# Optimization experiments

Measured on AMD Instinct MI355X. Metric: run time of the kernel, lower is better.

Reference implementation:

```python
import jax, jax.numpy as jnp
import numpy as np

N = 50000   # nodes
E = 800000  # edges (avg degree 16)
D = 128     # input feature dim
H = 128     # hidden dim
C = 10      # num classes
G = 16      # graphs in batch


def setup_inputs() -> dict:
    key = jax.random.key(0)
    ks = jax.random.split(key, 12)
    def w(k, shape):
        return jax.random.normal(k, shape, jnp.float32) / np.sqrt(shape[0]).astype(np.float32)
    return {
        "h": jax.random.normal(ks[0], (N, D), jnp.float32),
        "src": jax.random.randint(ks[1], (E,), 0, N, jnp.int32),
        "dst": jax.random.randint(ks[2], (E,), 0, N, jnp.int32),
        "graph_ids": jnp.sort(jax.random.randint(ks[3], (N,), 0, G, jnp.int32)),
        "W1a": w(ks[4], (D, H)), "b1a": jnp.zeros((H,), jnp.float32),
        "W2a": w(ks[5], (H, H)), "b2a": jnp.zeros((H,), jnp.float32),
        "W1b": w(ks[6], (H, H)), "b1b": jnp.zeros((H,), jnp.float32),
        "W2b": w(ks[7], (H, H)), "b2b": jnp.zeros((H,), jnp.float32),
        "Wc1": w(ks[8], (H, H)), "bc1": jnp.zeros((H,), jnp.float32),
        "Wc2": w(ks[9], (H, C)), "bc2": jnp.zeros((C,), jnp.float32),
    }


def _gin_layer(h, src, dst, W1, b1, W2, b2):
    # GIN aggregation, eps=0: z_i = h_i + sum_{j in N(i)} h_j
    agg = jax.ops.segment_sum(h[src], dst, num_segments=N)
    z = h + agg
    # 2-layer MLP apply function with relu activation ('relu' arg of GINLayer)
    z = jax.nn.relu(z @ W1 + b1)
    return jax.nn.relu(z @ W2 + b2)


def reference(h, src, dst, graph_ids, W1a, b1a, W2a, b2a,
              W1b, b1b, W2b, b2b, Wc1, bc1, Wc2, bc2):
    h = _gin_layer(h, src, dst, W1a, b1a, W2a, b2a)   # [N, H]
    h = _gin_layer(h, src, dst, W1b, b1b, W2b, b2b)   # [N, H]
    # dgl.mean_nodes over the batched graph
    sums = jax.ops.segment_sum(h, graph_ids, num_segments=G)                # [G, H]
    cnts = jax.ops.segment_sum(jnp.ones((N, 1), h.dtype), graph_ids, num_segments=G)
    h_g = sums / jnp.maximum(cnts, 1.0)
    # cls MLP: linear -> relu -> linear (logits)
    out = jax.nn.relu(h_g @ Wc1 + bc1) @ Wc2 + bc2    # [G, C]
    return out
```

## Files before the change

kernel.cpp:

```cpp
#include <hip/hip_runtime.h>
#include <stdint.h>

#define NN 50000
#define EE 800000
#define DD 128
#define GG 16
#define CC 10
#define NBK 196
#define BCH 4096
#define SMAX 5120

typedef unsigned short u16;
typedef __bf16 bf16x8 __attribute__((ext_vector_type(8)));
typedef float f32x4 __attribute__((ext_vector_type(4)));

__device__ inline u16 f2bf(float f) {
    unsigned u = __float_as_uint(f);
    u = u + 0x7fffu + ((u >> 16) & 1u);
    return (u16)(u >> 16);
}
__device__ inline unsigned pack2(float a, float b) {
    return (unsigned)f2bf(a) | ((unsigned)f2bf(b) << 16);
}
__device__ inline float bf2f(unsigned bits16) { return __uint_as_float(bits16 << 16); }
__device__ inline void acc8(float* a, uint4 v) {
    a[0] += __uint_as_float(v.x << 16); a[1] += __uint_as_float(v.x & 0xffff0000u);
    a[2] += __uint_as_float(v.y << 16); a[3] += __uint_as_float(v.y & 0xffff0000u);
    a[4] += __uint_as_float(v.z << 16); a[5] += __uint_as_float(v.z & 0xffff0000u);
    a[6] += __uint_as_float(v.w << 16); a[7] += __uint_as_float(v.w & 0xffff0000u);
}
__device__ inline void mand(uint4& v, int p) {
    unsigned m = p ? 0xffffffffu : 0u;
    v.x &= m; v.y &= m; v.z &= m; v.w &= m;
}

#define PZ (GG * DD)
#define PC (NN * DD / 4)
#define PW (4 * DD * DD)
#define PTOT (PZ + PC + PW)

__global__ void prep_kernel(const float* __restrict__ h,
                            const float* __restrict__ a, const float* __restrict__ b,
                            const float* __restrict__ c, const float* __restrict__ d,
                            int* __restrict__ zbase, u16* __restrict__ H0,
                            u16* __restrict__ wt) {
    int i = blockIdx.x * 256 + threadIdx.x;
    if (i < PZ) { zbase[i] = 0; return; }
    i -= PZ;
    if (i < PC) {
        int j = i * 4;
        float4 v = *(const float4*)(h + j);
        ushort4 o;
        o.x = f2bf(v.x); o.y = f2bf(v.y); o.z = f2bf(v.z); o.w = f2bf(v.w);
        *(ushort4*)(H0 + j) = o;
        return;
    }
    i -= PC;
    if (i < PW) {
        int m = i >> 14, r = i & 16383, k = r >> 7, j = r & 127;
        const float* W = (m == 0) ? a : (m == 1) ? b : (m == 2) ? c : d;
        wt[(m << 14) + (j << 7) + k] = f2bf(W[(k << 7) + j]);
    }
}

__global__ __launch_bounds__(256) void sortP1_kernel(const int* __restrict__ dst,
                                                     int* __restrict__ counts) {
    __shared__ int hist[NBK];
    int b = blockIdx.x, t = threadIdx.x;
    for (int i = t; i < NBK; i += 256) hist[i] = 0;
    __syncthreads();
    int e0 = b * BCH, e1 = min(e0 + BCH, EE);
    for (int e = e0 + t; e < e1; e += 256) atomicAdd(&hist[dst[e] >> 8], 1);
    __syncthreads();
    for (int i = t; i < NBK; i += 256) counts[b * NBK + i] = hist[i];
}

__global__ __launch_bounds__(256) void sortP2_kernel(int* __restrict__ counts,
                                                     int* __restrict__ bbase,
                                                     const int* __restrict__ gids,
                                                     int* __restrict__ gstart) {
    __shared__ int tmp[256];
    int t = threadIdx.x;
    if (t <= GG) {
        int lo = 0, hi = NN;
        while (lo < hi) { int mid = (lo + hi) >> 1; if (gids[mid] < t) lo = mid + 1; else hi = mid; }
        gstart[t] = lo;
    }
    int s = 0;
    if (t < NBK) {
        for (int b = 0; b < NBK; b++) {
            int c = counts[b * NBK + t];
            counts[b * NBK + t] = s;
            s += c;
        }
    }
    tmp[t] = (t < NBK) ? s : 0;
    __syncthreads();
    for (int off = 1; off < 256; off <<= 1) {
        int x = (t >= off) ? tmp[t - off] : 0;
        __syncthreads();
        tmp[t] += x;
        __syncthreads();
    }
    int base = tmp[t] - ((t < NBK) ? s : 0);
    if (t < NBK) {
        bbase[t] = base;
        for (int b = 0; b < NBK; b++) counts[b * NBK + t] += base;
    }
    if (t == NBK - 1) bbase[NBK] = tmp[t];
}

__global__ __launch_bounds__(256) void sortP3_kernel(const int* __restrict__ src,
                                                     const int* __restrict__ dst,
                                                     const int* __restrict__ counts,
                                                     int* __restrict__ epack) {
    __shared__ int curs[NBK];
    int b = blockIdx.x, t = threadIdx.x;
    for (int i = t; i < NBK; i += 256) curs[i] = counts[b * NBK + i];
    __syncthreads();
    int e0 = b * BCH, e1 = min(e0 + BCH, EE);
    for (int e = e0 + t; e < e1; e += 256) {
        int d = dst[e], s = src[e];
        int p = atomicAdd(&curs[d >> 8], 1);
        epack[p] = (s << 8) | (d & 255);
    }
}

__global__ __launch_bounds__(256) void sortP4_kernel(const int* __restrict__ epack,
                                                     const int* __restrict__ bbase,
                                                     int* __restrict__ offs,
                                                     int* __restrict__ ssrc) {
    __shared__ int hist[256];
    __shared__ int curs[256];
    __shared__ int stage[SMAX];
    int j = blockIdx.x, t = threadIdx.x;
    int n0 = j << 8;
    int b0 = bbase[j], b1 = bbase[j + 1];
    hist[t] = 0;
    __syncthreads();
    for (int e = b0 + t; e < b1; e += 256) atomicAdd(&hist[epack[e] & 255], 1);
    __syncthreads();
    int deg = hist[t];
    for (int off = 1; off < 256; off <<= 1) {
        int x = (t >= off) ? hist[t - off] : 0;
        __syncthreads();
        hist[t] += x;
        __syncthreads();
    }
    int loff = hist[t] - deg;
    curs[t] = loff;
    if (n0 + t <= NN) offs[n0 + t] = b0 + loff;
    __syncthreads();
    for (int e = b0 + t; e < b1; e += 256) {
        int pk = epack[e];
        int p = atomicAdd(&curs[pk & 255], 1);
        stage[p] = pk >> 8;
    }
    __syncthreads();
    int n = b1 - b0;
    for (int i = t; i < n; i += 256) ssrc[b0 + i] = stage[i];
}

__global__ __launch_bounds__(256) void agg_kernel(
    const u16* __restrict__ Hin, const int* __restrict__ offs,
    const int* __restrict__ ssrc, u16* __restrict__ Z) {
    int gid = blockIdx.x * 32 + (threadIdx.x >> 3);
    int lid = threadIdx.x & 7;
    if (gid >= 2 * NN) return;
    int node = gid >> 1;
    int foff = (gid & 1) * 64 + lid * 8;
    const u16* base = Hin + foff;

    float acc[8] = {0.f, 0.f, 0.f, 0.f, 0.f, 0.f, 0.f, 0.f};
    uint4 vs = *(const uint4*)(base + (size_t)node * DD);
    int e0 = offs[node], e1 = offs[node + 1];
    acc8(acc, vs);

    int nch = (e1 - e0 + 7) >> 3;
    if (nch > 0) {
        int elast = e1 - 1;
        int i0 = ssrc[e0];
        int i1 = ssrc[min(e0 + 1, elast)];
        int i2 = ssrc[min(e0 + 2, elast)];
        int i3 = ssrc[min(e0 + 3, elast)];
        int i4 = ssrc[min(e0 + 4, elast)];
        int i5 = ssrc[min(e0 + 5, elast)];
        int i6 = ssrc[min(e0 + 6, elast)];
        int i7 = ssrc[min(e0 + 7, elast)];
        int eb = e0;
        for (int c = 0; c < nch; c++) {
            int ebn = eb + 8;
            int n0 = i0, n1 = i1, n2 = i2, n3 = i3, n4 = i4, n5 = i5, n6 = i6, n7 = i7;
            if (c + 1 < nch) {
                n0 = ssrc[ebn];
                n1 = ssrc[min(ebn + 1, elast)];
                n2 = ssrc[min(ebn + 2, elast)];
                n3 = ssrc[min(ebn + 3, elast)];
                n4 = ssrc[min(ebn + 4, elast)];
                n5 = ssrc[min(ebn + 5, elast)];
                n6 = ssrc[min(ebn + 6, elast)];
                n7 = ssrc[min(ebn + 7, elast)];
            }
            uint4 v0 = *(const uint4*)(base + (size_t)i0 * DD);
            uint4 v1 = *(const uint4*)(base + (size_t)i1 * DD);
            uint4 v2 = *(const uint4*)(base + (size_t)i2 * DD);
            uint4 v3 = *(const uint4*)(base + (size_t)i3 * DD);
            uint4 v4 = *(const uint4*)(base + (size_t)i4 * DD);
            uint4 v5 = *(const uint4*)(base + (size_t)i5 * DD);
            uint4 v6 = *(const uint4*)(base + (size_t)i6 * DD);
            uint4 v7 = *(const uint4*)(base + (size_t)i7 * DD);
            mand(v1, eb + 1 < e1); mand(v2, eb + 2 < e1); mand(v3, eb + 3 < e1);
            mand(v4, eb + 4 < e1); mand(v5, eb + 5 < e1); mand(v6, eb + 6 < e1);
            mand(v7, eb + 7 < e1);
            acc8(acc, v0); acc8(acc, v1); acc8(acc, v2); acc8(acc, v3);
            acc8(acc, v4); acc8(acc, v5); acc8(acc, v6); acc8(acc, v7);
            i0 = n0; i1 = n1; i2 = n2; i3 = n3; i4 = n4; i5 = n5; i6 = n6; i7 = n7;
            eb = ebn;
        }
    }
    uint4 o;
    o.x = pack2(acc[0], acc[1]); o.y = pack2(acc[2], acc[3]);
    o.z = pack2(acc[4], acc[5]); o.w = pack2(acc[6], acc[7]);
    *(uint4*)(Z + (size_t)node * DD + foff) = o;
}

__global__ __launch_bounds__(256) void mlp_kernel(
    const u16* __restrict__ Zin, const u16* __restrict__ Wt1, const float* __restrict__ b1,
    const u16* __restrict__ Wt2, const float* __restrict__ b2,
    u16* __restrict__ Hout) {
    __shared__ u16 zb[64][136];
    const int wave = threadIdx.x >> 6;
    const int lane = threadIdx.x & 63;
    const int m16 = lane & 15;
    const int quad = lane >> 4;
    const int row0 = blockIdx.x * 64 + wave * 16;

#pragma unroll
    for (int p = 0; p < 4; p++) {
        int idx = p * 64 + lane;
        int r = idx >> 4, ch = idx & 15;
        if (row0 + r < NN)
            *(uint4*)&zb[wave * 16 + r][ch * 8] = *(const uint4*)(Zin + (size_t)(row0 + r) * DD + ch * 8);
    }

    bf16x8 afr[4];
#pragma unroll
    for (int kk = 0; kk < 4; kk++)
        afr[kk] = *(const bf16x8*)&zb[wave * 16 + m16][kk * 32 + quad * 8];
    f32x4 acc[8];
#pragma unroll
    for (int nt = 0; nt < 8; nt++) acc[nt] = (f32x4){0.f, 0.f, 0.f, 0.f};
#pragma unroll
    for (int kk = 0; kk < 4; kk++) {
#pragma unroll
        for (int nt = 0; nt < 8; nt++) {
            bf16x8 bfr = *(const bf16x8*)(Wt1 + ((nt * 16 + m16) << 7) + kk * 32 + quad * 8);
            acc[nt] = __builtin_amdgcn_mfma_f32_16x16x32_bf16(afr[kk], bfr, acc[nt], 0, 0, 0);
        }
    }
#pragma unroll
    for (int nt = 0; nt < 8; nt++) {
        int col = nt * 16 + m16;
        float bias = b1[col];
#pragma unroll
        for (int r = 0; r < 4; r++) {
            float yv = acc[nt][r] + bias;
            yv = yv > 0.f ? yv : 0.f;
            zb[wave * 16 + quad * 4 + r][col] = f2bf(yv);
        }
    }

#pragma unroll
    for (int kk = 0; kk < 4; kk++)
        afr[kk] = *(const bf16x8*)&zb[wave * 16 + m16][kk * 32 + quad * 8];
#pragma unroll
    for (int nt = 0; nt < 8; nt++) acc[nt] = (f32x4){0.f, 0.f, 0.f, 0.f};
#pragma unroll
    for (int kk = 0; kk < 4; kk++) {
#pragma unroll
        for (int nt = 0; nt < 8; nt++) {
            bf16x8 bfr = *(const bf16x8*)(Wt2 + ((nt * 16 + m16) << 7) + kk * 32 + quad * 8);
            acc[nt] = __builtin_amdgcn_mfma_f32_16x16x32_bf16(afr[kk], bfr, acc[nt], 0, 0, 0);
        }
    }
#pragma unroll
    for (int nt = 0; nt < 8; nt++) {
        int col = nt * 16 + m16;
        float bias = b2[col];
#pragma unroll
        for (int r = 0; r < 4; r++) {
            float ov = acc[nt][r] + bias;
            ov = ov > 0.f ? ov : 0.f;
            zb[wave * 16 + quad * 4 + r][col] = f2bf(ov);
        }
    }
#pragma unroll
    for (int p = 0; p < 4; p++) {
        int idx = p * 64 + lane;
        int r = idx >> 4, ch = idx & 15;
        if (row0 + r < NN)
            *(uint4*)(Hout + (size_t)(row0 + r) * DD + ch * 8) = *(const uint4*)&zb[wave * 16 + r][ch * 8];
    }
}

__global__ void pool_kernel(const u16* __restrict__ H2, const int* __restrict__ gstart,
                            float* __restrict__ pool) {
    int g = blockIdx.x >> 5, q = blockIdx.x & 31;
    int f = threadIdx.x;
    int s = gstart[g], e = gstart[g + 1];
    float sum = 0.f;
    for (int n = s + q; n < e; n += 32) sum += bf2f(H2[(size_t)n * DD + f]);
    atomicAdd(&pool[g * DD + f], sum);
}

__global__ void cls_kernel(const float* __restrict__ pool, const int* __restrict__ gstart,
                           const float* __restrict__ Wc1, const float* __restrict__ bc1,
                           const float* __restrict__ Wc2, const float* __restrict__ bc2,
                           float* __restrict__ out) {
    __shared__ float hg[128];
    __shared__ float y1[128];
    int g = blockIdx.x;
    int t = threadIdx.x;
    int cnt = gstart[g + 1] - gstart[g];
    float inv = 1.f / (float)(cnt > 1 ? cnt : 1);
    hg[t] = pool[g * DD + t] * inv;
    __syncthreads();
    float a = bc1[t];
    for (int k = 0; k < DD; k++) a += hg[k] * Wc1[k * DD + t];
    y1[t] = a > 0.f ? a : 0.f;
    __syncthreads();
    if (t < CC) {
        float o = bc2[t];
        for (int k = 0; k < DD; k++) o += y1[k] * Wc2[k * CC + t];
        out[g * CC + t] = o;
    }
}

extern "C" void kernel_launch(void* const* d_in, const int* in_sizes, int n_in,
                              void* d_out, int out_size, void* d_ws, size_t ws_size,
                              hipStream_t stream) {
    const float* h    = (const float*)d_in[0];
    const int*   src  = (const int*)d_in[1];
    const int*   dst  = (const int*)d_in[2];
    const int*   gids = (const int*)d_in[3];
    const float* W1a  = (const float*)d_in[4];
    const float* b1a  = (const float*)d_in[5];
    const float* W2a  = (const float*)d_in[6];
    const float* b2a  = (const float*)d_in[7];
    const float* W1b  = (const float*)d_in[8];
    const float* b1b  = (const float*)d_in[9];
    const float* W2b  = (const float*)d_in[10];
    const float* b2b  = (const float*)d_in[11];
    const float* Wc1  = (const float*)d_in[12];
    const float* bc1  = (const float*)d_in[13];
    const float* Wc2  = (const float*)d_in[14];
    const float* bc2  = (const float*)d_in[15];
    float* out = (float*)d_out;

    char* ws = (char*)d_ws;
    u16*   H0     = (u16*)(ws);
    u16*   H1     = (u16*)(ws + 12800000);
    u16*   H2     = (u16*)(ws + 25600000);
    u16*   Wt     = (u16*)(ws + 38400000);
    float* pool   = (float*)(ws + 38531072);
    int*   offs   = (int*)(ws + 38539264);
    int*   ssrc   = (int*)(ws + 38739268);
    int*   gstart = (int*)(ws + 41939268);
    int*   counts = (int*)(ws + 41939336);
    int*   bbase  = (int*)(ws + 42093000);
    int*   epack  = (int*)(ws + 42093792);
    u16*   Z1     = H2;
    u16*   Z2     = H0;

    prep_kernel<<<dim3((PTOT + 255) / 256), dim3(256), 0, stream>>>(h, W1a, W2a, W1b, W2b, (int*)pool, H0, Wt);
    sortP1_kernel<<<dim3(NBK), dim3(256), 0, stream>>>(dst, counts);
    sortP2_kernel<<<dim3(1), dim3(256), 0, stream>>>(counts, bbase, gids, gstart);
    sortP3_kernel<<<dim3(NBK), dim3(256), 0, stream>>>(src, dst, counts, epack);
    sortP4_kernel<<<dim3(NBK), dim3(256), 0, stream>>>(epack, bbase, offs, ssrc);
    agg_kernel<<<dim3((2 * NN + 31) / 32), dim3(256), 0, stream>>>(H0, offs, ssrc, Z1);
    mlp_kernel<<<dim3((NN + 63) / 64), dim3(256), 0, stream>>>(Z1, Wt, b1a, Wt + 16384, b2a, H1);
    agg_kernel<<<dim3((2 * NN + 31) / 32), dim3(256), 0, stream>>>(H1, offs, ssrc, Z2);
    mlp_kernel<<<dim3((NN + 63) / 64), dim3(256), 0, stream>>>(Z2, Wt + 32768, b1b, Wt + 49152, b2b, H2);
    pool_kernel<<<dim3(GG * 32), dim3(128), 0, stream>>>(H2, gstart, pool);
    cls_kernel<<<dim3(GG), dim3(128), 0, stream>>>(pool, gstart, Wc1, bc1, Wc2, bc2, out);
}
```

Measured before the change: 305.6 us.

## Fuse histogram into prep kernel, transpose counts for parallel scan, add nontemporal memops

The bucket histogram pass now runs in the same launch as the fp32-to-bf16 conversion and weight transpose, which removes one kernel launch and lets the two run concurrently. The counts table is stored bucket-major, so the single-block scan can split it into contiguous chunks per thread instead of serially walking 196 strided entries per thread. Bucket bases are then read directly from counts, and the separate bbase array is dropped. Nontemporal loads and stores are also used for streaming feature tensors in the prep, aggregation and MLP kernels, which risks losing L2 reuse where the next kernel reads the same data.

```diff
diff --git a/kernel.cpp b/kernel.cpp
--- a/kernel.cpp
+++ b/kernel.cpp
@@ -9,10 +9,14 @@
 #define NBK 196
 #define BCH 4096
 #define SMAX 5120
+#define FT (NBK * NBK)
+#define CHK 151
 
 typedef unsigned short u16;
 typedef __bf16 bf16x8 __attribute__((ext_vector_type(8)));
 typedef float f32x4 __attribute__((ext_vector_type(4)));
+typedef unsigned int u32x4 __attribute__((ext_vector_type(4)));
+typedef float fl4 __attribute__((ext_vector_type(4)));
 
 __device__ inline u16 f2bf(float f) {
     unsigned u = __float_as_uint(f);
@@ -33,23 +37,50 @@
     unsigned m = p ? 0xffffffffu : 0u;
     v.x &= m; v.y &= m; v.z &= m; v.w &= m;
 }
+__device__ inline void nt_store16(void* p, uint4 v) {
+    u32x4 x; x.x = v.x; x.y = v.y; x.z = v.z; x.w = v.w;
+    __builtin_nontemporal_store(x, (u32x4*)p);
+}
+__device__ inline uint4 nt_load16(const void* p) {
+    u32x4 x = __builtin_nontemporal_load((const u32x4*)p);
+    uint4 r; r.x = x.x; r.y = x.y; r.z = x.z; r.w = x.w;
+    return r;
+}
+__device__ inline float4 nt_loadf4(const float* p) {
+    fl4 x = __builtin_nontemporal_load((const fl4*)p);
+    float4 r; r.x = x.x; r.y = x.y; r.z = x.z; r.w = x.w;
+    return r;
+}
 
 #define PZ (GG * DD)
 #define PC (NN * DD / 4)
 #define PW (4 * DD * DD)
 #define PTOT (PZ + PC + PW)
-
-__global__ void prep_kernel(const float* __restrict__ h,
-                            const float* __restrict__ a, const float* __restrict__ b,
-                            const float* __restrict__ c, const float* __restrict__ d,
-                            int* __restrict__ zbase, u16* __restrict__ H0,
-                            u16* __restrict__ wt) {
-    int i = blockIdx.x * 256 + threadIdx.x;
+#define PBLK ((PTOT + 255) / 256)
+
+__global__ __launch_bounds__(256) void prepsort_kernel(
+    const float* __restrict__ h,
+    const float* __restrict__ a, const float* __restrict__ b,
+    const float* __restrict__ c, const float* __restrict__ d,
+    int* __restrict__ zbase, u16* __restrict__ H0, u16* __restrict__ wt,
+    const int* __restrict__ dst, int* __restrict__ counts) {
+    __shared__ int hist[NBK];
+    int blk = blockIdx.x, t = threadIdx.x;
+    if (blk < NBK) {
+        for (int i = t; i < NBK; i += 256) hist[i] = 0;
+        __syncthreads();
+        int e0 = blk * BCH, e1 = min(e0 + BCH, EE);
+        for (int e = e0 + t; e < e1; e += 256) atomicAdd(&hist[dst[e] >> 8], 1);
+        __syncthreads();
+        for (int i = t; i < NBK; i += 256) counts[i * NBK + blk] = hist[i];
+        return;
+    }
+    int i = (blk - NBK) * 256 + t;
     if (i < PZ) { zbase[i] = 0; return; }
     i -= PZ;
     if (i < PC) {
         int j = i * 4;
-        float4 v = *(const float4*)(h + j);
+        float4 v = nt_loadf4(h + j);
         ushort4 o;
         o.x = f2bf(v.x); o.y = f2bf(v.y); o.z = f2bf(v.z); o.w = f2bf(v.w);
         *(ushort4*)(H0 + j) = o;
@@ -63,20 +94,7 @@
     }
 }
 
-__global__ __launch_bounds__(256) void sortP1_kernel(const int* __restrict__ dst,
-                                                     int* __restrict__ counts) {
-    __shared__ int hist[NBK];
-    int b = blockIdx.x, t = threadIdx.x;
-    for (int i = t; i < NBK; i += 256) hist[i] = 0;
-    __syncthreads();
-    int e0 = b * BCH, e1 = min(e0 + BCH, EE);
-    for (int e = e0 + t; e < e1; e += 256) atomicAdd(&hist[dst[e] >> 8], 1);
-    __syncthreads();
-    for (int i = t; i < NBK; i += 256) counts[b * NBK + i] = hist[i];
-}
-
 __global__ __launch_bounds__(256) void sortP2_kernel(int* __restrict__ counts,
-                                                     int* __restrict__ bbase,
                                                      const int* __restrict__ gids,
                                                      int* __restrict__ gstart) {
     __shared__ int tmp[256];
@@ -86,15 +104,13 @@
         while (lo < hi) { int mid = (lo + hi) >> 1; if (gids[mid] < t) lo = mid + 1; else hi = mid; }
         gstart[t] = lo;
     }
+    int base = t * CHK;
     int s = 0;
-    if (t < NBK) {
-        for (int b = 0; b < NBK; b++) {
-            int c = counts[b * NBK + t];
-            counts[b * NBK + t] = s;
-            s += c;
-        }
-    }
-    tmp[t] = (t < NBK) ? s : 0;
+    for (int i = 0; i < CHK; i++) {
+        int idx = base + i;
+        if (idx < FT) s += counts[idx];
+    }
+    tmp[t] = s;
     __syncthreads();
     for (int off = 1; off < 256; off <<= 1) {
         int x = (t >= off) ? tmp[t - off] : 0;
@@ -102,12 +118,11 @@
         tmp[t] += x;
         __syncthreads();
     }
-    int base = tmp[t] - ((t < NBK) ? s : 0);
-    if (t < NBK) {
-        bbase[t] = base;
-        for (int b = 0; b < NBK; b++) counts[b * NBK + t] += base;
-    }
-    if (t == NBK - 1) bbase[NBK] = tmp[t];
+    int pre = tmp[t] - s;
+    for (int i = 0; i < CHK; i++) {
+        int idx = base + i;
+        if (idx < FT) { int cv = counts[idx]; counts[idx] = pre; pre += cv; }
+    }
 }
 
 __global__ __launch_bounds__(256) void sortP3_kernel(const int* __restrict__ src,
@@ -116,18 +131,18 @@
                                                      int* __restrict__ epack) {
     __shared__ int curs[NBK];
     int b = blockIdx.x, t = threadIdx.x;
-    for (int i = t; i < NBK; i += 256) curs[i] = counts[b * NBK + i];
+    for (int i = t; i < NBK; i += 256) curs[i] = counts[i * NBK + b];
     __syncthreads();
     int e0 = b * BCH, e1 = min(e0 + BCH, EE);
     for (int e = e0 + t; e < e1; e += 256) {
-        int d = dst[e], s = src[e];
-        int p = atomicAdd(&curs[d >> 8], 1);
-        epack[p] = (s << 8) | (d & 255);
+        int dd = dst[e], s = src[e];
+        int p = atomicAdd(&curs[dd >> 8], 1);
+        epack[p] = (s << 8) | (dd & 255);
     }
 }
 
 __global__ __launch_bounds__(256) void sortP4_kernel(const int* __restrict__ epack,
-                                                     const int* __restrict__ bbase,
+                                                     const int* __restrict__ counts,
                                                      int* __restrict__ offs,
                                                      int* __restrict__ ssrc) {
     __shared__ int hist[256];
@@ -135,7 +150,8 @@
     __shared__ int stage[SMAX];
     int j = blockIdx.x, t = threadIdx.x;
     int n0 = j << 8;
-    int b0 = bbase[j], b1 = bbase[j + 1];
+    int b0 = counts[j * NBK];
+    int b1 = (j < NBK - 1) ? counts[(j + 1) * NBK] : EE;
     hist[t] = 0;
     __syncthreads();
     for (int e = b0 + t; e < b1; e += 256) atomicAdd(&hist[epack[e] & 255], 1);
@@ -221,7 +237,7 @@
     uint4 o;
     o.x = pack2(acc[0], acc[1]); o.y = pack2(acc[2], acc[3]);
     o.z = pack2(acc[4], acc[5]); o.w = pack2(acc[6], acc[7]);
-    *(uint4*)(Z + (size_t)node * DD + foff) = o;
+    nt_store16(Z + (size_t)node * DD + foff, o);
 }
 
 __global__ __launch_bounds__(256) void mlp_kernel(
@@ -239,8 +255,10 @@
     for (int p = 0; p < 4; p++) {
         int idx = p * 64 + lane;
         int r = idx >> 4, ch = idx & 15;
-        if (row0 + r < NN)
-            *(uint4*)&zb[wave * 16 + r][ch * 8] = *(const uint4*)(Zin + (size_t)(row0 + r) * DD + ch * 8);
+        if (row0 + r < NN) {
+            uint4 v = nt_load16(Zin + (size_t)(row0 + r) * DD + ch * 8);
+            *(uint4*)&zb[wave * 16 + r][ch * 8] = v;
+        }
     }
 
     bf16x8 afr[4];
@@ -299,7 +317,7 @@
         int idx = p * 64 + lane;
         int r = idx >> 4, ch = idx & 15;
         if (row0 + r < NN)
-            *(uint4*)(Hout + (size_t)(row0 + r) * DD + ch * 8) = *(const uint4*)&zb[wave * 16 + r][ch * 8];
+            nt_store16(Hout + (size_t)(row0 + r) * DD + ch * 8, *(const uint4*)&zb[wave * 16 + r][ch * 8]);
     }
 }
 
@@ -367,16 +385,15 @@
     int*   ssrc   = (int*)(ws + 38739268);
     int*   gstart = (int*)(ws + 41939268);
     int*   counts = (int*)(ws + 41939336);
-    int*   bbase  = (int*)(ws + 42093000);
     int*   epack  = (int*)(ws + 42093792);
     u16*   Z1     = H2;
     u16*   Z2     = H0;
 
-    prep_kernel<<<dim3((PTOT + 255) / 256), dim3(256), 0, stream>>>(h, W1a, W2a, W1b, W2b, (int*)pool, H0, Wt);
-    sortP1_kernel<<<dim3(NBK), dim3(256), 0, stream>>>(dst, counts);
-    sortP2_kernel<<<dim3(1), dim3(256), 0, stream>>>(counts, bbase, gids, gstart);
+    prepsort_kernel<<<dim3(NBK + PBLK), dim3(256), 0, stream>>>(
+        h, W1a, W2a, W1b, W2b, (int*)pool, H0, Wt, dst, counts);
+    sortP2_kernel<<<dim3(1), dim3(256), 0, stream>>>(counts, gids, gstart);
     sortP3_kernel<<<dim3(NBK), dim3(256), 0, stream>>>(src, dst, counts, epack);
-    sortP4_kernel<<<dim3(NBK), dim3(256), 0, stream>>>(epack, bbase, offs, ssrc);
+    sortP4_kernel<<<dim3(NBK), dim3(256), 0, stream>>>(epack, counts, offs, ssrc);
     agg_kernel<<<dim3((2 * NN + 31) / 32), dim3(256), 0, stream>>>(H0, offs, ssrc, Z1);
     mlp_kernel<<<dim3((NN + 63) / 64), dim3(256), 0, stream>>>(Z1, Wt, b1a, Wt + 16384, b2a, H1);
     agg_kernel<<<dim3((2 * NN + 31) / 32), dim3(256), 0, stream>>>(H1, offs, ssrc, Z2);
```

After: 376.9 us. +23.3%, slower.
